# Kernel tuning notes

Measured on AMD Instinct MI355X. Metric: run time of the kernel, lower is better.

Reference implementation:

```python
import jax, jax.numpy as jnp
import numpy as np

B, T, RES, C = 4, 8, 32, 128
TSP, SPLIT = 4, 4
NH_BRANCH = 4  # num_heads // 2 per branch
HID = 4 * C


def layer_norm(x, w, b, eps=1e-5):
    mu = x.mean(-1, keepdims=True)
    var = ((x - mu) ** 2).mean(-1, keepdims=True)
    return (x - mu) * jax.lax.rsqrt(var + eps) * w + b


def dwconv3d(x, w, b):
    # x: (Bw, C, Tsp, Hsp, Wsp); w: (C, 1, 3, 3, 3) depthwise
    y = jax.lax.conv_general_dilated(
        x, w, (1, 1, 1), 'SAME',
        dimension_numbers=('NCDHW', 'OIDHW', 'NCDHW'),
        feature_group_count=x.shape[1])
    return y + b[None, :, None, None, None]


def lepe_attention(q, k, v, conv_w, conv_b, Tsp, Hsp, Wsp, nh, Tt, H, W):
    Bq, L, Cc = q.shape
    hd = Cc // nh
    win = Tsp * Hsp * Wsp
    scale = float(hd) ** -0.5

    def to_win(z):
        z = z.reshape(Bq, Tt // Tsp, Tsp, H // Hsp, Hsp, W // Wsp, Wsp, Cc)
        z = z.transpose(0, 1, 3, 5, 2, 4, 6, 7).reshape(-1, win, nh, hd)
        return z.transpose(0, 2, 1, 3)

    qw = to_win(q) * scale
    kw = to_win(k)
    # v windows as (Bw, C, Tsp, Hsp, Wsp) for the depthwise-conv LePE
    vw5 = v.reshape(Bq, Tt // Tsp, Tsp, H // Hsp, Hsp, W // Wsp, Wsp, Cc)
    vw5 = vw5.transpose(0, 1, 3, 5, 7, 2, 4, 6).reshape(-1, Cc, Tsp, Hsp, Wsp)
    lepe = dwconv3d(vw5, conv_w, conv_b)

    def heads(z5):
        return z5.reshape(-1, nh, hd, win).transpose(0, 1, 3, 2)

    vh, lepeh = heads(vw5), heads(lepe)
    attn = jax.nn.softmax(jnp.einsum('bnqd,bnkd->bnqk', qw, kw), axis=-1)
    out = jnp.einsum('bnqk,bnkd->bnqd', attn, vh) + lepeh
    # windows -> video token order (T, H, W)
    out = out.transpose(0, 2, 1, 3).reshape(
        Bq, Tt // Tsp, H // Hsp, W // Wsp, Tsp, Hsp, Wsp, Cc)
    out = out.transpose(0, 1, 4, 2, 5, 3, 6, 7).reshape(Bq, L, Cc)
    return out


def setup_inputs() -> dict:
    key = jax.random.key(0)
    ks = jax.random.split(key, 16)
    L = T * RES * RES
    h = C // 2
    p = lambda k, s: jax.random.normal(k, s, dtype=jnp.float32) * 0.02
    return {
        'x': jax.random.normal(ks[0], (B, L, C), dtype=jnp.float32),
        'norm1_w': jnp.ones((C,), jnp.float32),
        'norm1_b': jnp.zeros((C,), jnp.float32),
        'qkv_w': p(ks[1], (3 * C, C)),
        'conv_w0': p(ks[2], (h, 1, 3, 3, 3)),
        'conv_b0': jnp.zeros((h,), jnp.float32),
        'conv_w1': p(ks[3], (h, 1, 3, 3, 3)),
        'conv_b1': jnp.zeros((h,), jnp.float32),
        'proj_w': p(ks[4], (C, C)),
        'proj_b': jnp.zeros((C,), jnp.float32),
        'norm2_w': jnp.ones((C,), jnp.float32),
        'norm2_b': jnp.zeros((C,), jnp.float32),
        'fc1_w': p(ks[5], (HID, C)),
        'fc1_b': jnp.zeros((HID,), jnp.float32),
        'fc2_w': p(ks[6], (C, HID)),
        'fc2_b': jnp.zeros((C,), jnp.float32),
    }


def reference(x, norm1_w, norm1_b, qkv_w, conv_w0, conv_b0, conv_w1, conv_b1,
              proj_w, proj_b, norm2_w, norm2_b, fc1_w, fc1_b, fc2_w, fc2_b):
    img = layer_norm(x, norm1_w, norm1_b)
    qkv = img @ qkv_w.T  # (B, L, 3C), split order q, k, v
    q, k, v = jnp.split(qkv, 3, axis=-1)
    h = C // 2
    # branch 0 (idx=0): H_sp = reso, W_sp = split_size
    x1 = lepe_attention(q[..., :h], k[..., :h], v[..., :h], conv_w0, conv_b0,
                        TSP, RES, SPLIT, NH_BRANCH, T, RES, RES)
    # branch 1 (idx=1): H_sp = split_size, W_sp = reso
    x2 = lepe_attention(q[..., h:], k[..., h:], v[..., h:], conv_w1, conv_b1,
                        TSP, SPLIT, RES, NH_BRANCH, T, RES, RES)
    att = jnp.concatenate([x1, x2], axis=2) @ proj_w.T + proj_b
    x = x + att
    y = layer_norm(x, norm2_w, norm2_b)
    y = jax.nn.gelu(y @ fc1_w.T + fc1_b, approximate=False) @ fc2_w.T + fc2_b
    return x + y
```

## Files before the change

kernel.cpp:

```cpp
#include <hip/hip_runtime.h>
#include <math.h>

namespace {
constexpr int C_ = 128;
constexpr int BL = 32768;
constexpr int LS = 140;

typedef __attribute__((ext_vector_type(4))) float f32x4;
typedef __attribute__((ext_vector_type(4))) _Float16 f16x4;
typedef __attribute__((ext_vector_type(8))) _Float16 f16x8;
typedef __attribute__((ext_vector_type(2))) __fp16 hf2;

#if __has_builtin(__builtin_amdgcn_exp2f)
#define EXP2F(x) __builtin_amdgcn_exp2f(x)
#else
#define EXP2F(x) exp2f(x)
#endif
}

__global__ __launch_bounds__(256) void k_cvt(
    const float* __restrict__ qkvw, const float* __restrict__ pw,
    const float* __restrict__ f1w,  const float* __restrict__ f2w,
    const float* __restrict__ cw0,  const float* __restrict__ cw1,
    _Float16* __restrict__ wqh, _Float16* __restrict__ pwh,
    _Float16* __restrict__ w1h, _Float16* __restrict__ w2h,
    float* __restrict__ lepw)
{
  int i = blockIdx.x * 256 + threadIdx.x;
  if (i < 49152) {
    float v = qkvw[i];
    if (i < 16384) v *= 0.360673762f;
    wqh[i] = (_Float16)v;
  }
  else if (i < 65536)  pwh[i - 49152] = (_Float16)pw[i - 49152];
  else if (i < 131072) w1h[i - 65536] = (_Float16)f1w[i - 65536];
  else if (i < 196608) w2h[i - 131072] = (_Float16)f2w[i - 131072];
  else if (i < 200064) {
    int j = i - 196608;
    int br = j / 1728, r = j % 1728, widx = r >> 6, ch = r & 63;
    lepw[j] = (br ? cw1 : cw0)[ch * 27 + widx];
  }
}

__global__ __launch_bounds__(512) void k_ln_qkv(
    const float* __restrict__ x,
    const float* __restrict__ nw,
    const float* __restrict__ nb,
    const _Float16* __restrict__ wqh,
    _Float16* __restrict__ qh, _Float16* __restrict__ kh, _Float16* __restrict__ vh)
{
  __shared__ _Float16 xs[64][LS];
  __shared__ _Float16 qt[64][LS];
  __shared__ _Float16 wbuf[128][LS];
  const int tid = threadIdx.x;
  const int row0 = blockIdx.x << 6;
  const int bb = row0 >> 13, t = (row0 >> 10) & 7, h0 = (row0 >> 5) & 31;
  const int tb = t >> 2, t_in = t & 3;

  {
    const int r = tid >> 3, j = tid & 7;
    const float* xp = x + (size_t)(row0 + r) * C_ + j * 16;
    float v[16];
#pragma unroll
    for (int i = 0; i < 4; ++i) {
      float4 u = ((const float4*)xp)[i];
      v[i*4+0] = u.x; v[i*4+1] = u.y; v[i*4+2] = u.z; v[i*4+3] = u.w;
    }
    float s1 = 0.f, s2 = 0.f;
#pragma unroll
    for (int i = 0; i < 16; ++i) { s1 += v[i]; s2 += v[i] * v[i]; }
    s1 += __shfl_down(s1, 4, 8); s1 += __shfl_down(s1, 2, 8); s1 += __shfl_down(s1, 1, 8);
    s2 += __shfl_down(s2, 4, 8); s2 += __shfl_down(s2, 2, 8); s2 += __shfl_down(s2, 1, 8);
    float mu = __shfl(s1, 0, 8) * (1.f / 128.f);
    float ms = __shfl(s2, 0, 8) * (1.f / 128.f);
    float rstd = rsqrtf(ms - mu * mu + 1e-5f);
#pragma unroll
    for (int i = 0; i < 16; ++i) {
      int c = j * 16 + i;
      xs[r][c] = (_Float16)((v[i] - mu) * rstd * nw[c] + nb[c]);
    }
  }
  __syncthreads();

  const int lane = tid & 63, wave = tid >> 6;
  const int mq = wave & 3, nh = wave >> 2;
  const int m0 = mq << 4, mi = lane & 15, quad = lane >> 4;

  f16x8 afr[4];
#pragma unroll
  for (int kt = 0; kt < 4; ++kt)
    afr[kt] = *(const f16x8*)&xs[m0 + mi][kt * 32 + quad * 8];

  for (int g = 0; g < 3; ++g) {
#pragma unroll
    for (int it = 0; it < 4; ++it) {
      int id = it * 512 + tid;
      int r = id >> 4, c8 = id & 15;
      *(uint4*)&wbuf[r][c8 * 8] = *(const uint4*)(wqh + (size_t)(g * 128 + r) * 128 + c8 * 8);
    }
    __syncthreads();

    f32x4 acc[4];
#pragma unroll
    for (int nt = 0; nt < 4; ++nt) acc[nt] = (f32x4){0.f, 0.f, 0.f, 0.f};
#pragma unroll
    for (int nt = 0; nt < 4; ++nt) {
      int wrow = (nh * 4 + nt) * 16 + mi;
#pragma unroll
      for (int kt = 0; kt < 4; ++kt) {
        f16x8 bfr = *(const f16x8*)&wbuf[wrow][kt * 32 + quad * 8];
        acc[nt] = __builtin_amdgcn_mfma_f32_16x16x32_f16(afr[kt], bfr, acc[nt], 0, 0, 0);
      }
    }
#pragma unroll
    for (int nt = 0; nt < 4; ++nt) {
      int n = (nh * 4 + nt) * 16 + mi;
#pragma unroll
      for (int rr = 0; rr < 4; ++rr)
        qt[m0 + quad * 4 + rr][n] = (_Float16)acc[nt][rr];
    }
    __syncthreads();

    _Float16* G = (g == 0) ? qh : (g == 1) ? kh : vh;
#pragma unroll
    for (int it = 0; it < 2; ++it) {
      int u = it * 512 + tid;
      if (u < 512) {
        int half = u & 1, p = (u >> 1) & 7, head = (u >> 4) & 3, sb = u >> 6;
        int token = (p >> 2) * 32 + sb * 4 + (p & 3);
        uint4 d = *(const uint4*)&qt[token][head * 16 + half * 8];
        int win = bb * 16 + tb * 8 + sb;
        int pos = t_in * 128 + h0 * 4 + p;
        *(uint4*)(G + ((size_t)(head * 64 + win) * 512 + pos) * 16 + half * 8) = d;
      } else {
        int u2 = u - 512;
        int half = u2 & 1, pin = (u2 >> 1) & 63, head = u2 >> 7;
        uint4 d = *(const uint4*)&qt[pin][64 + head * 16 + half * 8];
        int win = bb * 16 + tb * 8 + (h0 >> 2);
        int pos = t_in * 128 + (h0 & 3) * 32 + pin;
        *(uint4*)(G + ((size_t)((4 + head) * 64 + win) * 512 + pos) * 16 + half * 8) = d;
      }
    }
    __syncthreads();
  }
}

__global__ __launch_bounds__(512) void k_attn(
    const _Float16* __restrict__ qh,
    const _Float16* __restrict__ kh,
    const _Float16* __restrict__ vh,
    const float* __restrict__ lepw,
    const float* __restrict__ cb0,
    const float* __restrict__ cb1,
    _Float16* __restrict__ attnh)
{
  __shared__ _Float16 Ks[512][20];
  __shared__ _Float16 Vs[512][20];
  __shared__ _Float16 Vt[16][520];

  const int tid = threadIdx.x;
  const int bid = blockIdx.x;
  const int br = bid >> 8, wi = (bid >> 2) & 63, head = bid & 3;
  const int b = wi >> 4, tb = (wi >> 3) & 1, sb = wi & 7;
  const int coff = br * 64 + head * 16;
  const int Hsp = br ? 4 : 32, Wsp = br ? 32 : 4;
  const float* cb = br ? cb1 : cb0;
  const size_t base = ((size_t)(br * 4 + head) * 64 + wi) * 512 * 16;

  auto token_of = [&](int p) -> int {
    int t_in = p >> 7;
    int rem = p & 127;
    int h, w;
    if (br == 0) { h = rem >> 2;            w = sb * 4 + (rem & 3); }
    else         { h = sb * 4 + (rem >> 5); w = rem & 31; }
    return ((b * 8 + tb * 4 + t_in) << 10) + (h << 5) + w;
  };

  {
    const int r = tid;
    const _Float16* kp = kh + base + r * 16;
    const _Float16* vp = vh + base + r * 16;
    f16x8 k0 = *(const f16x8*)kp;
    f16x8 k1 = *(const f16x8*)(kp + 8);
    f16x8 v0 = *(const f16x8*)vp;
    f16x8 v1 = *(const f16x8*)(vp + 8);
    *(f16x4*)&Ks[r][0]  = (f16x4){k0[0], k0[1], k0[2], k0[3]};
    *(f16x4*)&Ks[r][4]  = (f16x4){k0[4], k0[5], k0[6], k0[7]};
    *(f16x4*)&Ks[r][8]  = (f16x4){k1[0], k1[1], k1[2], k1[3]};
    *(f16x4*)&Ks[r][12] = (f16x4){k1[4], k1[5], k1[6], k1[7]};
    *(f16x4*)&Vs[r][0]  = (f16x4){v0[0], v0[1], v0[2], v0[3]};
    *(f16x4*)&Vs[r][4]  = (f16x4){v0[4], v0[5], v0[6], v0[7]};
    *(f16x4*)&Vs[r][8]  = (f16x4){v1[0], v1[1], v1[2], v1[3]};
    *(f16x4*)&Vs[r][12] = (f16x4){v1[4], v1[5], v1[6], v1[7]};
#pragma unroll
    for (int d = 0; d < 8; ++d) { Vt[d][r] = v0[d]; Vt[d + 8][r] = v1[d]; }
  }

  const int lane = tid & 63, wave = tid >> 6;
  const int mi = lane & 15, quad = lane >> 4;

  int qtok[4];
  f16x4 qfr[4];
#pragma unroll
  for (int qi = 0; qi < 4; ++qi) {
    int q = (wave * 4 + qi) * 16 + mi;
    qtok[qi] = token_of(q);
    qfr[qi] = *(const f16x4*)(qh + base + q * 16 + quad * 4);
  }
  __syncthreads();

  f32x4 acc[4];
  float l[4];
#pragma unroll
  for (int qi = 0; qi < 4; ++qi) { acc[qi] = (f32x4){0.f,0.f,0.f,0.f}; l[qi] = 0.f; }

  const hf2 one2 = {(__fp16)1.f, (__fp16)1.f};

  for (int kt = 0; kt < 32; ++kt) {
    const int kb = kt << 4;
    f16x4 kfr = *(const f16x4*)&Ks[kb + mi][quad * 4];
    f16x4 vfr = *(const f16x4*)&Vt[mi][kb + quad * 4];
#pragma unroll
    for (int qi = 0; qi < 4; ++qi) {
      f32x4 s = __builtin_amdgcn_mfma_f32_16x16x16f16(kfr, qfr[qi], (f32x4){0.f,0.f,0.f,0.f}, 0, 0, 0);
      float p0 = EXP2F(s[0]);
      float p1 = EXP2F(s[1]);
      float p2 = EXP2F(s[2]);
      float p3 = EXP2F(s[3]);
      hf2 plo = __builtin_amdgcn_cvt_pkrtz(p0, p1);
      hf2 phi = __builtin_amdgcn_cvt_pkrtz(p2, p3);
#if __has_builtin(__builtin_amdgcn_fdot2)
      l[qi] = __builtin_amdgcn_fdot2(plo, one2, l[qi], false);
      l[qi] = __builtin_amdgcn_fdot2(phi, one2, l[qi], false);
#else
      l[qi] += (p0 + p1) + (p2 + p3);
#endif
      union { struct { hf2 lo, hi; } h; f16x4 v; } u;
      u.h.lo = plo; u.h.hi = phi;
      acc[qi] = __builtin_amdgcn_mfma_f32_16x16x16f16(vfr, u.v, acc[qi], 0, 0, 0);
    }
  }

#pragma unroll
  for (int qi = 0; qi < 4; ++qi) {
    float lq = l[qi];
    lq += __shfl_xor(lq, 16, 64);
    lq += __shfl_xor(lq, 32, 64);
    float inv = 1.f / lq;

    const int q = (wave * 4 + qi) * 16 + mi;
    int t_in = q >> 7, rem = q & 127;
    int h_in, w_in;
    if (br == 0) { h_in = rem >> 2; w_in = rem & 3; }
    else         { h_in = rem >> 5; w_in = rem & 31; }
    float4 lep = *(const float4*)(cb + head * 16 + quad * 4);
    for (int dz = 0; dz < 3; ++dz) {
      int tz = t_in + dz - 1; if ((unsigned)tz >= 4u) continue;
      for (int dy = 0; dy < 3; ++dy) {
        int ty = h_in + dy - 1; if ((unsigned)ty >= (unsigned)Hsp) continue;
        for (int dx = 0; dx < 3; ++dx) {
          int tx = w_in + dx - 1; if ((unsigned)tx >= (unsigned)Wsp) continue;
          int np = (tz * Hsp + ty) * Wsp + tx;
          int widx = (dz * 3 + dy) * 3 + dx;
          float4 w4 = *(const float4*)(lepw + ((br * 27 + widx) << 6) + head * 16 + quad * 4);
          f16x4 vv = *(const f16x4*)&Vs[np][quad * 4];
          lep.x += w4.x * (float)vv[0];
          lep.y += w4.y * (float)vv[1];
          lep.z += w4.z * (float)vv[2];
          lep.w += w4.w * (float)vv[3];
        }
      }
    }
    f16x4 ov;
    ov[0] = (_Float16)(acc[qi][0] * inv + lep.x);
    ov[1] = (_Float16)(acc[qi][1] * inv + lep.y);
    ov[2] = (_Float16)(acc[qi][2] * inv + lep.z);
    ov[3] = (_Float16)(acc[qi][3] * inv + lep.w);
    *(f16x4*)(attnh + (size_t)qtok[qi] * 128 + coff + quad * 4) = ov;
  }
}

__global__ __launch_bounds__(512) void k_pm(
    const _Float16* __restrict__ attnh,
    const _Float16* __restrict__ pwh,
    const float* __restrict__ pb,
    const float* __restrict__ x,
    const float* __restrict__ nw,
    const float* __restrict__ nb,
    const _Float16* __restrict__ w1h,
    const float* __restrict__ f1b,
    const _Float16* __restrict__ w2h,
    const float* __restrict__ f2b,
    float* __restrict__ out)
{
  __shared__ _Float16 as_[64][LS];
  __shared__ _Float16 wbuf[128][LS];
  __shared__ _Float16 xrb[64][LS];
  const int tid = threadIdx.x;
  const int row0 = blockIdx.x << 6;
  const int lane = tid & 63, wave = tid >> 6;
  const int mi = lane & 15, quad = lane >> 4;

#pragma unroll
  for (int it = 0; it < 2; ++it) {
    int id = it * 512 + tid;
    int r = id >> 4, c8 = id & 15;
    *(uint4*)&as_[r][c8 * 8] = *(const uint4*)(attnh + (size_t)(row0 + r) * 128 + c8 * 8);
  }
#pragma unroll
  for (int it = 0; it < 4; ++it) {
    int id = it * 512 + tid;
    int r = id >> 4, c8 = id & 15;
    *(uint4*)&wbuf[r][c8 * 8] = *(const uint4*)(pwh + (size_t)r * 128 + c8 * 8);
  }
  __syncthreads();

  {
    const int mq = wave & 3, nh = wave >> 2;
    const int m0 = mq << 4;

    f16x8 afr[4];
#pragma unroll
    for (int kt = 0; kt < 4; ++kt)
      afr[kt] = *(const f16x8*)&as_[m0 + mi][kt * 32 + quad * 8];

    f32x4 acc[4];
#pragma unroll
    for (int nt = 0; nt < 4; ++nt) acc[nt] = (f32x4){0.f, 0.f, 0.f, 0.f};
#pragma unroll
    for (int nt = 0; nt < 4; ++nt) {
      int wrow = (nh * 4 + nt) * 16 + mi;
#pragma unroll
      for (int kt = 0; kt < 4; ++kt) {
        f16x8 bfr = *(const f16x8*)&wbuf[wrow][kt * 32 + quad * 8];
        acc[nt] = __builtin_amdgcn_mfma_f32_16x16x32_f16(afr[kt], bfr, acc[nt], 0, 0, 0);
      }
    }
#pragma unroll
    for (int nt = 0; nt < 4; ++nt) {
      int n = (nh * 4 + nt) * 16 + mi;
      float bb = pb[n];
#pragma unroll
      for (int rr = 0; rr < 4; ++rr)
        xrb[m0 + quad * 4 + rr][n] = (_Float16)(acc[nt][rr] + bb);
    }
  }
  __syncthreads();

#pragma unroll
  for (int it = 0; it < 2; ++it) {
    int id = it * 512 + tid;
    int r = id >> 4, c8 = id & 15;
    f16x8 v = *(const f16x8*)&xrb[r][c8 * 8];
    const float* xp = x + (size_t)(row0 + r) * 128 + c8 * 8;
    float4 xa = *(const float4*)xp;
    float4 xb = *(const float4*)(xp + 4);
    f16x8 o;
    o[0] = (_Float16)((float)v[0] + xa.x); o[1] = (_Float16)((float)v[1] + xa.y);
    o[2] = (_Float16)((float)v[2] + xa.z); o[3] = (_Float16)((float)v[3] + xa.w);
    o[4] = (_Float16)((float)v[4] + xb.x); o[5] = (_Float16)((float)v[5] + xb.y);
    o[6] = (_Float16)((float)v[6] + xb.z); o[7] = (_Float16)((float)v[7] + xb.w);
    *(f16x8*)&xrb[r][c8 * 8] = o;
  }
  __syncthreads();

  {
    const int r = tid >> 3, j = tid & 7;
    float v[16];
#pragma unroll
    for (int i = 0; i < 2; ++i) {
      f16x8 u = *(const f16x8*)&xrb[r][j * 16 + i * 8];
#pragma unroll
      for (int k = 0; k < 8; ++k) v[i * 8 + k] = (float)u[k];
    }
    float s1 = 0.f, s2 = 0.f;
#pragma unroll
    for (int i = 0; i < 16; ++i) { s1 += v[i]; s2 += v[i] * v[i]; }
    s1 += __shfl_down(s1, 4, 8); s1 += __shfl_down(s1, 2, 8); s1 += __shfl_down(s1, 1, 8);
    s2 += __shfl_down(s2, 4, 8); s2 += __shfl_down(s2, 2, 8); s2 += __shfl_down(s2, 1, 8);
    float mu = __shfl(s1, 0, 8) * (1.f / 128.f);
    float ms = __shfl(s2, 0, 8) * (1.f / 128.f);
    float rstd = rsqrtf(ms - mu * mu + 1e-5f);
#pragma unroll
    for (int i = 0; i < 16; ++i) {
      int c = j * 16 + i;
      as_[r][c] = (_Float16)((v[i] - mu) * rstd * nw[c] + nb[c]);
    }
  }
  __syncthreads();

  const int mt = wave & 3, hh = wave >> 2;
  const int tok0 = mt << 4;

  f16x8 bx[4];
#pragma unroll
  for (int kt = 0; kt < 4; ++kt)
    bx[kt] = *(const f16x8*)&as_[tok0 + mi][kt * 32 + quad * 8];

  f32x4 oacc[8];
#pragma unroll
  for (int o = 0; o < 8; ++o) oacc[o] = (f32x4){0.f, 0.f, 0.f, 0.f};

  auto gelu = [](float h) -> float {
    return h * __frcp_rn(1.f + EXP2F(-2.4554774f * h));
  };

  for (int ng = 0; ng < 4; ++ng) {
#pragma unroll
    for (int it = 0; it < 4; ++it) {
      int id = it * 512 + tid;
      int r = id >> 4, c8 = id & 15;
      *(uint4*)&wbuf[r][c8 * 8] = *(const uint4*)(w1h + (size_t)(ng * 128 + r) * 128 + c8 * 8);
    }
    __syncthreads();

    f32x4 hacc[4];
#pragma unroll
    for (int t = 0; t < 4; ++t) hacc[t] = (f32x4){0.f, 0.f, 0.f, 0.f};
#pragma unroll
    for (int t = 0; t < 4; ++t) {
      int hrow = hh * 64 + t * 16 + mi;
#pragma unroll
      for (int kt = 0; kt < 4; ++kt) {
        f16x8 wfr = *(const f16x8*)&wbuf[hrow][kt * 32 + quad * 8];
        hacc[t] = __builtin_amdgcn_mfma_f32_16x16x32_f16(wfr, bx[kt], hacc[t], 0, 0, 0);
      }
    }
    f16x4 ph[4];
#pragma unroll
    for (int t = 0; t < 4; ++t) {
      float4 bj = *(const float4*)(f1b + ng * 128 + hh * 64 + t * 16 + quad * 4);
      ph[t][0] = (_Float16)gelu(hacc[t][0] + bj.x);
      ph[t][1] = (_Float16)gelu(hacc[t][1] + bj.y);
      ph[t][2] = (_Float16)gelu(hacc[t][2] + bj.z);
      ph[t][3] = (_Float16)gelu(hacc[t][3] + bj.w);
    }
    __syncthreads();

#pragma unroll
    for (int it = 0; it < 4; ++it) {
      int id = it * 512 + tid;
      int r = id >> 4, c8 = id & 15;
      *(uint4*)&wbuf[r][c8 * 8] = *(const uint4*)(w2h + (size_t)r * 512 + ng * 128 + c8 * 8);
    }
    __syncthreads();

#pragma unroll
    for (int o = 0; o < 8; ++o) {
#pragma unroll
      for (int t = 0; t < 4; ++t) {
        f16x4 wfr = *(const f16x4*)&wbuf[o * 16 + mi][(hh * 4 + t) * 16 + quad * 4];
        oacc[o] = __builtin_amdgcn_mfma_f32_16x16x16f16(wfr, ph[t], oacc[o], 0, 0, 0);
      }
    }
    __syncthreads();
  }

  float* rbuf = (float*)wbuf;
  if (hh == 1) {
#pragma unroll
    for (int o = 0; o < 8; ++o)
#pragma unroll
      for (int k = 0; k < 4; ++k)
        rbuf[(o * 4 + k) * 256 + mt * 64 + lane] = oacc[o][k];
  }
  __syncthreads();
  if (hh == 0) {
#pragma unroll
    for (int o = 0; o < 8; ++o)
#pragma unroll
      for (int k = 0; k < 4; ++k)
        oacc[o][k] += rbuf[(o * 4 + k) * 256 + mt * 64 + lane];

#pragma unroll
    for (int o = 0; o < 8; ++o) {
      int row = row0 + tok0 + mi;
      int cb4 = o * 16 + quad * 4;
      float4 bo = *(const float4*)(f2b + cb4);
      f16x4 res = *(const f16x4*)&xrb[tok0 + mi][cb4];
      float4 ov;
      ov.x = oacc[o][0] + bo.x + (float)res[0];
      ov.y = oacc[o][1] + bo.y + (float)res[1];
      ov.z = oacc[o][2] + bo.z + (float)res[2];
      ov.w = oacc[o][3] + bo.w + (float)res[3];
      *(float4*)(out + (size_t)row * C_ + cb4) = ov;
    }
  }
}

extern "C" void kernel_launch(void* const* d_in, const int* in_sizes, int n_in,
                              void* d_out, int out_size, void* d_ws, size_t ws_size,
                              hipStream_t stream)
{
  const float* x    = (const float*)d_in[0];
  const float* n1w  = (const float*)d_in[1];
  const float* n1b  = (const float*)d_in[2];
  const float* qkvw = (const float*)d_in[3];
  const float* cw0  = (const float*)d_in[4];
  const float* cb0  = (const float*)d_in[5];
  const float* cw1  = (const float*)d_in[6];
  const float* cb1  = (const float*)d_in[7];
  const float* pw   = (const float*)d_in[8];
  const float* pb   = (const float*)d_in[9];
  const float* n2w  = (const float*)d_in[10];
  const float* n2b  = (const float*)d_in[11];
  const float* f1w  = (const float*)d_in[12];
  const float* f1b  = (const float*)d_in[13];
  const float* f2w  = (const float*)d_in[14];
  const float* f2b  = (const float*)d_in[15];

  char* ws = (char*)d_ws;
  _Float16* qh    = (_Float16*)ws;
  _Float16* kh    = (_Float16*)(ws +  8388608);
  _Float16* vh    = (_Float16*)(ws + 16777216);
  _Float16* attnh = (_Float16*)(ws + 25165824);
  _Float16* wqh   = (_Float16*)(ws + 33554432);
  _Float16* pwh   = (_Float16*)(ws + 33652736);
  _Float16* w1h   = (_Float16*)(ws + 33685504);
  _Float16* w2h   = (_Float16*)(ws + 33816576);
  float*    lepw  = (float*)   (ws + 33947648);

  k_cvt   <<<782,      256, 0, stream>>>(qkvw, pw, f1w, f2w, cw0, cw1,
                                         wqh, pwh, w1h, w2h, lepw);
  k_ln_qkv<<<BL / 64,  512, 0, stream>>>(x, n1w, n1b, wqh, qh, kh, vh);
  k_attn  <<<512,      512, 0, stream>>>(qh, kh, vh, lepw, cb0, cb1, attnh);
  k_pm    <<<BL / 64,  512, 0, stream>>>(attnh, pwh, pb, x, n2w, n2b,
                                         w1h, f1b, w2h, f2b, (float*)d_out);
}
```

Before: 175.5 us.

## Halve k_pm weight staging buffer to raise occupancy with split weight passes

The shared weight buffer in the fused proj+MLP kernel shrinks from 128 to 64 rows, so the projection, fc1 and fc2 weights are streamed in two half-tiles with extra barriers. The hidden-unit assignment per wave is remapped to fit the halves, and the cross-wave reduction is split across two shared buffers. Launch bounds now request 6 blocks per CU. The aim is to cut LDS use so more blocks fit per CU and hide memory latency, at the cost of twice as many barriers and global reload steps.

```diff
diff --git a/kernel.cpp b/kernel.cpp
--- a/kernel.cpp
+++ b/kernel.cpp
@@ -280,7 +280,7 @@
   }
 }
 
-__global__ __launch_bounds__(512) void k_pm(
+__global__ __launch_bounds__(512, 6) void k_pm(
     const _Float16* __restrict__ attnh,
     const _Float16* __restrict__ pwh,
     const float* __restrict__ pb,
@@ -294,7 +294,7 @@
     float* __restrict__ out)
 {
   __shared__ _Float16 as_[64][LS];
-  __shared__ _Float16 wbuf[128][LS];
+  __shared__ _Float16 wbuf[64][LS];
   __shared__ _Float16 xrb[64][LS];
   const int tid = threadIdx.x;
   const int row0 = blockIdx.x << 6;
@@ -308,7 +308,7 @@
     *(uint4*)&as_[r][c8 * 8] = *(const uint4*)(attnh + (size_t)(row0 + r) * 128 + c8 * 8);
   }
 #pragma unroll
-  for (int it = 0; it < 4; ++it) {
+  for (int it = 0; it < 2; ++it) {
     int id = it * 512 + tid;
     int r = id >> 4, c8 = id & 15;
     *(uint4*)&wbuf[r][c8 * 8] = *(const uint4*)(pwh + (size_t)r * 128 + c8 * 8);
@@ -326,24 +326,44 @@
 
     f32x4 acc[4];
 #pragma unroll
-    for (int nt = 0; nt < 4; ++nt) acc[nt] = (f32x4){0.f, 0.f, 0.f, 0.f};
-#pragma unroll
-    for (int nt = 0; nt < 4; ++nt) {
-      int wrow = (nh * 4 + nt) * 16 + mi;
+    for (int j = 0; j < 4; ++j) acc[j] = (f32x4){0.f, 0.f, 0.f, 0.f};
+
+#pragma unroll
+    for (int nt = 0; nt < 2; ++nt) {
+      int wrow = nh * 32 + nt * 16 + mi;
 #pragma unroll
       for (int kt = 0; kt < 4; ++kt) {
         f16x8 bfr = *(const f16x8*)&wbuf[wrow][kt * 32 + quad * 8];
         acc[nt] = __builtin_amdgcn_mfma_f32_16x16x32_f16(afr[kt], bfr, acc[nt], 0, 0, 0);
       }
     }
-#pragma unroll
-    for (int nt = 0; nt < 4; ++nt) {
-      int n = (nh * 4 + nt) * 16 + mi;
-      float bb = pb[n];
-#pragma unroll
-      for (int rr = 0; rr < 4; ++rr)
-        xrb[m0 + quad * 4 + rr][n] = (_Float16)(acc[nt][rr] + bb);
-    }
+    __syncthreads();
+#pragma unroll
+    for (int it = 0; it < 2; ++it) {
+      int id = it * 512 + tid;
+      int r = id >> 4, c8 = id & 15;
+      *(uint4*)&wbuf[r][c8 * 8] = *(const uint4*)(pwh + (size_t)(64 + r) * 128 + c8 * 8);
+    }
+    __syncthreads();
+#pragma unroll
+    for (int nt = 0; nt < 2; ++nt) {
+      int wrow = nh * 32 + nt * 16 + mi;
+#pragma unroll
+      for (int kt = 0; kt < 4; ++kt) {
+        f16x8 bfr = *(const f16x8*)&wbuf[wrow][kt * 32 + quad * 8];
+        acc[2 + nt] = __builtin_amdgcn_mfma_f32_16x16x32_f16(afr[kt], bfr, acc[2 + nt], 0, 0, 0);
+      }
+    }
+#pragma unroll
+    for (int h2 = 0; h2 < 2; ++h2)
+#pragma unroll
+      for (int nt = 0; nt < 2; ++nt) {
+        int n = h2 * 64 + nh * 32 + nt * 16 + mi;
+        float bb = pb[n];
+#pragma unroll
+        for (int rr = 0; rr < 4; ++rr)
+          xrb[m0 + quad * 4 + rr][n] = (_Float16)(acc[h2 * 2 + nt][rr] + bb);
+      }
   }
   __syncthreads();
 
@@ -406,76 +426,84 @@
   };
 
   for (int ng = 0; ng < 4; ++ng) {
-#pragma unroll
-    for (int it = 0; it < 4; ++it) {
-      int id = it * 512 + tid;
-      int r = id >> 4, c8 = id & 15;
-      *(uint4*)&wbuf[r][c8 * 8] = *(const uint4*)(w1h + (size_t)(ng * 128 + r) * 128 + c8 * 8);
-    }
-    __syncthreads();
-
-    f32x4 hacc[4];
-#pragma unroll
-    for (int t = 0; t < 4; ++t) hacc[t] = (f32x4){0.f, 0.f, 0.f, 0.f};
-#pragma unroll
-    for (int t = 0; t < 4; ++t) {
-      int hrow = hh * 64 + t * 16 + mi;
-#pragma unroll
-      for (int kt = 0; kt < 4; ++kt) {
-        f16x8 wfr = *(const f16x8*)&wbuf[hrow][kt * 32 + quad * 8];
-        hacc[t] = __builtin_amdgcn_mfma_f32_16x16x32_f16(wfr, bx[kt], hacc[t], 0, 0, 0);
-      }
-    }
     f16x4 ph[4];
 #pragma unroll
-    for (int t = 0; t < 4; ++t) {
-      float4 bj = *(const float4*)(f1b + ng * 128 + hh * 64 + t * 16 + quad * 4);
-      ph[t][0] = (_Float16)gelu(hacc[t][0] + bj.x);
-      ph[t][1] = (_Float16)gelu(hacc[t][1] + bj.y);
-      ph[t][2] = (_Float16)gelu(hacc[t][2] + bj.z);
-      ph[t][3] = (_Float16)gelu(hacc[t][3] + bj.w);
-    }
-    __syncthreads();
-
-#pragma unroll
-    for (int it = 0; it < 4; ++it) {
-      int id = it * 512 + tid;
-      int r = id >> 4, c8 = id & 15;
-      *(uint4*)&wbuf[r][c8 * 8] = *(const uint4*)(w2h + (size_t)r * 512 + ng * 128 + c8 * 8);
-    }
-    __syncthreads();
-
-#pragma unroll
-    for (int o = 0; o < 8; ++o) {
-#pragma unroll
-      for (int t = 0; t < 4; ++t) {
-        f16x4 wfr = *(const f16x4*)&wbuf[o * 16 + mi][(hh * 4 + t) * 16 + quad * 4];
-        oacc[o] = __builtin_amdgcn_mfma_f32_16x16x16f16(wfr, ph[t], oacc[o], 0, 0, 0);
-      }
-    }
-    __syncthreads();
-  }
-
-  float* rbuf = (float*)wbuf;
+    for (int hf = 0; hf < 2; ++hf) {
+#pragma unroll
+      for (int it = 0; it < 2; ++it) {
+        int id = it * 512 + tid;
+        int r = id >> 4, c8 = id & 15;
+        *(uint4*)&wbuf[r][c8 * 8] =
+            *(const uint4*)(w1h + (size_t)(ng * 128 + hf * 64 + r) * 128 + c8 * 8);
+      }
+      __syncthreads();
+#pragma unroll
+      for (int t = 0; t < 2; ++t) {
+        int hrow = hh * 32 + t * 16 + mi;
+        f32x4 hacc = (f32x4){0.f, 0.f, 0.f, 0.f};
+#pragma unroll
+        for (int kt = 0; kt < 4; ++kt) {
+          f16x8 wfr = *(const f16x8*)&wbuf[hrow][kt * 32 + quad * 8];
+          hacc = __builtin_amdgcn_mfma_f32_16x16x32_f16(wfr, bx[kt], hacc, 0, 0, 0);
+        }
+        float4 bj = *(const float4*)(f1b + ng * 128 + hf * 64 + hh * 32 + t * 16 + quad * 4);
+        ph[hf * 2 + t][0] = (_Float16)gelu(hacc[0] + bj.x);
+        ph[hf * 2 + t][1] = (_Float16)gelu(hacc[1] + bj.y);
+        ph[hf * 2 + t][2] = (_Float16)gelu(hacc[2] + bj.z);
+        ph[hf * 2 + t][3] = (_Float16)gelu(hacc[3] + bj.w);
+      }
+      __syncthreads();
+    }
+
+#pragma unroll
+    for (int hf2 = 0; hf2 < 2; ++hf2) {
+#pragma unroll
+      for (int it = 0; it < 2; ++it) {
+        int id = it * 512 + tid;
+        int r = id >> 4, c8 = id & 15;
+        *(uint4*)&wbuf[r][c8 * 8] =
+            *(const uint4*)(w2h + (size_t)(hf2 * 64 + r) * 512 + ng * 128 + c8 * 8);
+      }
+      __syncthreads();
+#pragma unroll
+      for (int o2 = 0; o2 < 4; ++o2) {
+#pragma unroll
+        for (int j = 0; j < 4; ++j) {
+          int kti = (j >> 1) * 4 + hh * 2 + (j & 1);
+          f16x4 wfr = *(const f16x4*)&wbuf[o2 * 16 + mi][kti * 16 + quad * 4];
+          oacc[hf2 * 4 + o2] =
+              __builtin_amdgcn_mfma_f32_16x16x16f16(wfr, ph[j], oacc[hf2 * 4 + o2], 0, 0, 0);
+        }
+      }
+      __syncthreads();
+    }
+  }
+
+  float* rbufA = (float*)as_;
+  float* rbufB = (float*)wbuf;
   if (hh == 1) {
 #pragma unroll
-    for (int o = 0; o < 8; ++o)
-#pragma unroll
-      for (int k = 0; k < 4; ++k)
-        rbuf[(o * 4 + k) * 256 + mt * 64 + lane] = oacc[o][k];
+    for (int o = 0; o < 4; ++o)
+#pragma unroll
+      for (int k = 0; k < 4; ++k) {
+        rbufA[(o * 4 + k) * 256 + mt * 64 + lane] = oacc[o][k];
+        rbufB[(o * 4 + k) * 256 + mt * 64 + lane] = oacc[4 + o][k];
+      }
   }
   __syncthreads();
   if (hh == 0) {
 #pragma unroll
-    for (int o = 0; o < 8; ++o)
-#pragma unroll
-      for (int k = 0; k < 4; ++k)
-        oacc[o][k] += rbuf[(o * 4 + k) * 256 + mt * 64 + lane];
+    for (int o = 0; o < 4; ++o)
+#pragma unroll
+      for (int k = 0; k < 4; ++k) {
+        oacc[o][k]     += rbufA[(o * 4 + k) * 256 + mt * 64 + lane];
+        oacc[4 + o][k] += rbufB[(o * 4 + k) * 256 + mt * 64 + lane];
+      }
 
 #pragma unroll
     for (int o = 0; o < 8; ++o) {
       int row = row0 + tok0 + mi;
-      int cb4 = o * 16 + quad * 4;
+      int cb4 = (o >> 2) * 64 + (o & 3) * 16 + quad * 4;
       float4 bo = *(const float4*)(f2b + cb4);
       f16x4 res = *(const f16x4*)&xrb[tok0 + mi][cb4];
       float4 ov;
```

Result: slower. 192.1 us (+9.5%).
